# Optimization experiments

Measured on AMD Instinct MI355X. Metric: run time of the kernel, lower is better.

## Reference

```python
import jax, jax.numpy as jnp
import numpy as np

D_MODEL = 768
HEADS = 12
HEAD_DIM = D_MODEL // HEADS


def setup_inputs() -> dict:
    key = jax.random.key(0)
    ks = jax.random.split(key, 5)
    B, L = 4, 2048
    x = jax.random.normal(ks[0], (B, L, D_MODEL), dtype=jnp.float32)
    # torch nn.Linear init scale ~ 1/sqrt(fan_in); use small random weights
    s = 1.0 / np.sqrt(D_MODEL)
    W_qkv = jax.random.uniform(ks[1], (D_MODEL, 3 * D_MODEL), jnp.float32, -s, s)
    b_qkv = jax.random.uniform(ks[2], (3 * D_MODEL,), jnp.float32, -s, s)
    W_out = jax.random.uniform(ks[3], (D_MODEL, D_MODEL), jnp.float32, -s, s)
    b_out = jax.random.uniform(ks[4], (D_MODEL,), jnp.float32, -s, s)
    return {"x": x, "W_qkv": W_qkv, "b_qkv": b_qkv, "W_out": W_out, "b_out": b_out}


def reference(x, W_qkv, b_qkv, W_out, b_out):
    B, L, D = x.shape
    scale = jnp.sqrt(jnp.float32(HEAD_DIM))
    # qkv projection: [B, L, 3*D] -> [3, B, heads, L, head_dim]
    qkv = (x @ W_qkv + b_qkv).reshape(B, L, 3, HEADS, HEAD_DIM)
    qkv = jnp.transpose(qkv, (2, 0, 3, 1, 4))
    q, k, v = qkv[0], qkv[1], qkv[2]
    # full materialized attention, no mask
    scores = jnp.einsum("bhld,bhmd->bhlm", q, k) / scale  # [B, H, L, L]
    attn = jax.nn.softmax(scores, axis=-1)
    out = jnp.einsum("bhlm,bhmd->bhld", attn, v)  # [B, H, L, head_dim]
    out = jnp.transpose(out, (0, 2, 1, 3)).reshape(B, L, D)
    return out @ W_out + b_out
```

## Files before the change

### kernel.cpp

```cpp
#include <hip/hip_runtime.h>
#include <cmath>

typedef __bf16 bf16_t;
typedef __bf16 bf16x8 __attribute__((ext_vector_type(8)));
typedef __bf16 bf16x4 __attribute__((ext_vector_type(4)));
typedef short s16x4 __attribute__((ext_vector_type(4)));
typedef float f32x4 __attribute__((ext_vector_type(4)));

#define MFMA(a, b, c) __builtin_amdgcn_mfma_f32_16x16x32_bf16((a), (b), (c), 0, 0, 0)
#if __has_builtin(__builtin_amdgcn_mfma_f32_16x16x16_bf16)
#define MFMA16(a, b, c) __builtin_amdgcn_mfma_f32_16x16x16_bf16((a), (b), (c), 0, 0, 0)
#else
#define MFMA16(a, b, c)                                                              \
  __builtin_amdgcn_mfma_f32_16x16x16bf16_1k(__builtin_bit_cast(s16x4, (bf16x4)(a)), \
                                            __builtin_bit_cast(s16x4, (bf16x4)(b)), (c), 0, 0, 0)
#endif

static constexpr int D = 768;
static constexpr int L = 2048;
static constexpr int NB = 4;
static constexpr int NH = 12;
static constexpr int HD = 64;
static constexpr int M = 8192;
static constexpr int NQKV = 2304;
#define QSCALE 0.18033688011112042f

__device__ __forceinline__ void glds16(const bf16_t* g, bf16_t* l) {
  __builtin_amdgcn_global_load_lds((const __attribute__((address_space(1))) void*)g,
                                   (__attribute__((address_space(3))) void*)l, 16, 0, 0);
}

__global__ __launch_bounds__(256) void cvt_bf16_kernel(const float* __restrict__ in,
                                                       bf16_t* __restrict__ out, int n8) {
  int g = blockIdx.x * 256 + threadIdx.x;
  if (g >= n8) return;
  const float4* p = (const float4*)in + (size_t)g * 2;
  float4 a = p[0], b = p[1];
  bf16x8 v = {(__bf16)a.x, (__bf16)a.y, (__bf16)a.z, (__bf16)a.w,
              (__bf16)b.x, (__bf16)b.y, (__bf16)b.z, (__bf16)b.w};
  *(bf16x8*)(out + (size_t)g * 8) = v;
}

__global__ __launch_bounds__(256) void transpose_cvt_kernel(const float* __restrict__ in,
                                                            bf16_t* __restrict__ out,
                                                            int rows, int cols) {
  __shared__ float t[32][33];
  int c0 = blockIdx.x * 32, r0 = blockIdx.y * 32;
  int tx = threadIdx.x, ty = threadIdx.y;
  for (int i = ty; i < 32; i += 8) t[i][tx] = in[(size_t)(r0 + i) * cols + c0 + tx];
  __syncthreads();
  for (int i = ty; i < 32; i += 8) out[(size_t)(c0 + i) * rows + r0 + tx] = (__bf16)t[tx][i];
}

__global__ __launch_bounds__(256) void gemm_qkv_kernel(const bf16_t* __restrict__ A,
                                                       const bf16_t* __restrict__ Bt,
                                                       const float* __restrict__ bias,
                                                       bf16_t* __restrict__ Qo,
                                                       bf16_t* __restrict__ Ko,
                                                       bf16_t* __restrict__ Vto) {
  __shared__ __align__(16) bf16_t As[128 * 32];
  __shared__ __align__(16) bf16_t Bs[128 * 32];
  const int tid = threadIdx.x;
  const int wave = tid >> 6, lane = tid & 63;
  const int quad = lane >> 4, l16 = lane & 15;
  const int wm = (wave >> 1) * 64, wn = (wave & 1) * 64;
  const int tm = blockIdx.x * 128, tn = blockIdx.y * 128;
  const int lr = tid >> 2, lc = (tid & 3) * 8;
  const bf16_t* Ag = A + (size_t)(tm + lr) * D + lc;
  const bf16_t* Bg = Bt + (size_t)(tn + lr) * D + lc;
  bf16_t* lA0 = &As[wave * 512];
  bf16_t* lA1 = &As[2048 + wave * 512];
  bf16_t* lB0 = &Bs[wave * 512];
  bf16_t* lB1 = &Bs[2048 + wave * 512];
  f32x4 acc[4][4] = {};
  for (int kt = 0; kt < D; kt += 32) {
    __syncthreads();
    glds16(Ag + kt, lA0);
    glds16(Ag + (size_t)64 * D + kt, lA1);
    glds16(Bg + kt, lB0);
    glds16(Bg + (size_t)64 * D + kt, lB1);
    __syncthreads();
    bf16x8 af[4], bfr[4];
#pragma unroll
    for (int i = 0; i < 4; i++) af[i] = *(const bf16x8*)&As[(wm + i * 16 + l16) * 32 + quad * 8];
#pragma unroll
    for (int j = 0; j < 4; j++) bfr[j] = *(const bf16x8*)&Bs[(wn + j * 16 + l16) * 32 + quad * 8];
#pragma unroll
    for (int i = 0; i < 4; i++)
#pragma unroll
      for (int j = 0; j < 4; j++) acc[i][j] = MFMA(af[i], bfr[j], acc[i][j]);
  }
#pragma unroll
  for (int i = 0; i < 4; i++)
#pragma unroll
    for (int j = 0; j < 4; j++) {
      int n = tn + wn + j * 16 + l16;
      float bn = bias[n];
      int which = n / 768, rem = n - which * 768;
      int h = rem >> 6, d = rem & 63;
      int m0 = tm + wm + i * 16 + quad * 4;
      int b0 = m0 >> 11, l0 = m0 & 2047;
      int bh = b0 * NH + h;
      if (which == 2) {
        int l6 = l0 & 63;
        int lp = (l0 & ~63) | (((l6 >> 2) & 3) * 16) | ((l6 >> 4) * 4);
        bf16x4 w;
#pragma unroll
        for (int r2 = 0; r2 < 4; r2++) w[r2] = (__bf16)(acc[i][j][r2] + bn);
        *(bf16x4*)&Vto[((size_t)bh * HD + d) * L + lp] = w;
      } else if (which == 0) {
#pragma unroll
        for (int r2 = 0; r2 < 4; r2++)
          Qo[((size_t)bh * L + l0 + r2) * HD + d] = (__bf16)((acc[i][j][r2] + bn) * QSCALE);
      } else {
#pragma unroll
        for (int r2 = 0; r2 < 4; r2++)
          Ko[((size_t)bh * L + l0 + r2) * HD + d] = (__bf16)(acc[i][j][r2] + bn);
      }
    }
}

__global__ __launch_bounds__(256) void attn_kernel(const bf16_t* __restrict__ Q,
                                                   const bf16_t* __restrict__ K,
                                                   const bf16_t* __restrict__ Vt,
                                                   bf16_t* __restrict__ O) {
  __shared__ __align__(16) bf16_t Ks[64][72];
  __shared__ __align__(16) bf16_t Vs[64][72];
  const int tid = threadIdx.x;
  const int wave = tid >> 6, lane = tid & 63;
  const int quad = lane >> 4, l16 = lane & 15;
  const int bh = blockIdx.y;
  const int q0 = blockIdx.x * 128 + wave * 32;
  const bf16_t* Kb = K + (size_t)bh * L * HD;
  const bf16_t* Vb = Vt + (size_t)bh * HD * L;
  bf16x8 bq[2][2];
#pragma unroll
  for (int g = 0; g < 2; g++) {
    const bf16_t* Qp = Q + ((size_t)bh * L + q0 + g * 16 + l16) * HD + quad * 8;
    bq[g][0] = *(const bf16x8*)Qp;
    bq[g][1] = *(const bf16x8*)(Qp + 32);
  }
  f32x4 oacc[2][4] = {};
  float lacc[2] = {0.f, 0.f};
  const int st = tid >> 3, sc = (tid & 7) * 8;
  bf16x8 pk0 = *(const bf16x8*)(Kb + (size_t)st * HD + sc);
  bf16x8 pk1 = *(const bf16x8*)(Kb + (size_t)(st + 32) * HD + sc);
  bf16x8 pv0 = *(const bf16x8*)(Vb + (size_t)st * L + sc);
  bf16x8 pv1 = *(const bf16x8*)(Vb + (size_t)(st + 32) * L + sc);
  for (int j = 0; j < L / 64; j++) {
    __syncthreads();
    *(bf16x8*)&Ks[st][sc] = pk0;
    *(bf16x8*)&Ks[st + 32][sc] = pk1;
    *(bf16x8*)&Vs[st][sc] = pv0;
    *(bf16x8*)&Vs[st + 32][sc] = pv1;
    __syncthreads();
    if (j + 1 < L / 64) {
      int kv0n = (j + 1) * 64;
      pk0 = *(const bf16x8*)(Kb + (size_t)(kv0n + st) * HD + sc);
      pk1 = *(const bf16x8*)(Kb + (size_t)(kv0n + st + 32) * HD + sc);
      pv0 = *(const bf16x8*)(Vb + (size_t)st * L + kv0n + sc);
      pv1 = *(const bf16x8*)(Vb + (size_t)(st + 32) * L + kv0n + sc);
    }
    f32x4 s[2][4];
#pragma unroll
    for (int fn = 0; fn < 4; fn++) {
      bf16x8 ak0 = *(const bf16x8*)&Ks[fn * 16 + l16][quad * 8];
      bf16x8 ak1 = *(const bf16x8*)&Ks[fn * 16 + l16][32 + quad * 8];
#pragma unroll
      for (int g = 0; g < 2; g++) {
        f32x4 z = {};
        z = MFMA(ak0, bq[g][0], z);
        s[g][fn] = MFMA(ak1, bq[g][1], z);
      }
    }
    bf16x4 pb[2][4];
#pragma unroll
    for (int g = 0; g < 2; g++)
#pragma unroll
      for (int fn = 0; fn < 4; fn++) {
        float e0 = exp2f(s[g][fn][0]), e1 = exp2f(s[g][fn][1]);
        float e2 = exp2f(s[g][fn][2]), e3 = exp2f(s[g][fn][3]);
        lacc[g] += (e0 + e1) + (e2 + e3);
        bf16x4 w = {(__bf16)e0, (__bf16)e1, (__bf16)e2, (__bf16)e3};
        pb[g][fn] = w;
      }
#pragma unroll
    for (int fd = 0; fd < 4; fd++)
#pragma unroll
      for (int t = 0; t < 2; t++) {
        bf16x8 av2 = *(const bf16x8*)&Vs[fd * 16 + l16][quad * 16 + t * 8];
        bf16x4 av0 = {av2[0], av2[1], av2[2], av2[3]};
        bf16x4 av1 = {av2[4], av2[5], av2[6], av2[7]};
#pragma unroll
        for (int g = 0; g < 2; g++) {
          oacc[g][fd] = MFMA16(av0, pb[g][2 * t], oacc[g][fd]);
          oacc[g][fd] = MFMA16(av1, pb[g][2 * t + 1], oacc[g][fd]);
        }
      }
  }
  const int b = bh / NH, h = bh - b * NH;
#pragma unroll
  for (int g = 0; g < 2; g++) {
    float ls = lacc[g];
    ls += __shfl_xor(ls, 16, 64);
    ls += __shfl_xor(ls, 32, 64);
    float rinv = 1.f / ls;
    int row = q0 + g * 16 + l16;
    bf16_t* Op = O + ((size_t)(b * L + row)) * D + h * HD;
#pragma unroll
    for (int fd = 0; fd < 4; fd++) {
      bf16x4 w;
#pragma unroll
      for (int r = 0; r < 4; r++) w[r] = (__bf16)(oacc[g][fd][r] * rinv);
      *(bf16x4*)(Op + fd * 16 + quad * 4) = w;
    }
  }
}

__global__ __launch_bounds__(256) void gemm_out_kernel(const bf16_t* __restrict__ A,
                                                       const bf16_t* __restrict__ Bt,
                                                       const float* __restrict__ bias,
                                                       float* __restrict__ Cg) {
  __shared__ __align__(16) bf16_t As[128 * 32];
  __shared__ __align__(16) bf16_t Bs[128 * 32];
  const int tid = threadIdx.x;
  const int wave = tid >> 6, lane = tid & 63;
  const int quad = lane >> 4, l16 = lane & 15;
  const int wm = (wave >> 1) * 64, wn = (wave & 1) * 64;
  const int tm = blockIdx.x * 128, tn = blockIdx.y * 128;
  const int lr = tid >> 2, lc = (tid & 3) * 8;
  const bf16_t* Ag = A + (size_t)(tm + lr) * D + lc;
  const bf16_t* Bg = Bt + (size_t)(tn + lr) * D + lc;
  bf16_t* lA0 = &As[wave * 512];
  bf16_t* lA1 = &As[2048 + wave * 512];
  bf16_t* lB0 = &Bs[wave * 512];
  bf16_t* lB1 = &Bs[2048 + wave * 512];
  f32x4 acc[4][4] = {};
  for (int kt = 0; kt < D; kt += 32) {
    __syncthreads();
    glds16(Ag + kt, lA0);
    glds16(Ag + (size_t)64 * D + kt, lA1);
    glds16(Bg + kt, lB0);
    glds16(Bg + (size_t)64 * D + kt, lB1);
    __syncthreads();
    bf16x8 af[4], bfr[4];
#pragma unroll
    for (int i = 0; i < 4; i++) af[i] = *(const bf16x8*)&As[(wm + i * 16 + l16) * 32 + quad * 8];
#pragma unroll
    for (int j = 0; j < 4; j++) bfr[j] = *(const bf16x8*)&Bs[(wn + j * 16 + l16) * 32 + quad * 8];
#pragma unroll
    for (int i = 0; i < 4; i++)
#pragma unroll
      for (int j = 0; j < 4; j++) acc[i][j] = MFMA(af[i], bfr[j], acc[i][j]);
  }
#pragma unroll
  for (int i = 0; i < 4; i++)
#pragma unroll
    for (int j = 0; j < 4; j++) {
      int n = tn + wn + j * 16 + l16;
      float bn = bias[n];
#pragma unroll
      for (int r2 = 0; r2 < 4; r2++) {
        int m = tm + wm + i * 16 + quad * 4 + r2;
        Cg[(size_t)m * D + n] = acc[i][j][r2] + bn;
      }
    }
}

extern "C" void kernel_launch(void* const* d_in, const int* in_sizes, int n_in,
                              void* d_out, int out_size, void* d_ws, size_t ws_size,
                              hipStream_t stream) {
  const float* x = (const float*)d_in[0];
  const float* Wqkv = (const float*)d_in[1];
  const float* bqkv = (const float*)d_in[2];
  const float* Wout = (const float*)d_in[3];
  const float* bout = (const float*)d_in[4];
  float* out = (float*)d_out;

  bf16_t* xb = (bf16_t*)d_ws;
  bf16_t* wqT = xb + (size_t)M * D;
  bf16_t* woT = wqT + (size_t)NQKV * D;
  bf16_t* Qb = woT + (size_t)D * D;
  bf16_t* Kb = Qb + (size_t)M * D;
  bf16_t* Vtb = Kb + (size_t)M * D;
  bf16_t* Ob = Vtb + (size_t)M * D;

  cvt_bf16_kernel<<<(M * D / 8 + 255) / 256, 256, 0, stream>>>(x, xb, M * D / 8);
  transpose_cvt_kernel<<<dim3(NQKV / 32, D / 32), dim3(32, 8), 0, stream>>>(Wqkv, wqT, D, NQKV);
  transpose_cvt_kernel<<<dim3(D / 32, D / 32), dim3(32, 8), 0, stream>>>(Wout, woT, D, D);
  gemm_qkv_kernel<<<dim3(M / 128, NQKV / 128), 256, 0, stream>>>(xb, wqT, bqkv, Qb, Kb, Vtb);
  attn_kernel<<<dim3(L / 128, NB * NH), 256, 0, stream>>>(Qb, Kb, Vtb, Ob);
  gemm_out_kernel<<<dim3(M / 128, D / 128), 256, 0, stream>>>(Ob, woT, bout, out);
}
```

Before: 244.9 us.

## Load K/V fragments directly from global memory, dropping LDS staging and barriers

The attention kernel no longer stages K and V tiles through shared memory with two __syncthreads per iteration. Each wave now loads its MFMA operand fragments for K and V^T straight from global memory into registers. It also switches exp2f to the raw hardware exp2 builtin and requests 3 blocks per CU in launch_bounds. This removes the barrier and LDS round-trip cost, but each of the four waves now fetches the same K/V data separately, so it relies on L1/L2 hits and exposes global load latency with no explicit prefetch.

```diff
diff --git a/kernel.cpp b/kernel.cpp
--- a/kernel.cpp
+++ b/kernel.cpp
@@ -15,6 +15,8 @@
   __builtin_amdgcn_mfma_f32_16x16x16bf16_1k(__builtin_bit_cast(s16x4, (bf16x4)(a)), \
                                             __builtin_bit_cast(s16x4, (bf16x4)(b)), (c), 0, 0, 0)
 #endif
+
+#define EXP2(x) __builtin_amdgcn_exp2f(x)
 
 static constexpr int D = 768;
 static constexpr int L = 2048;
@@ -120,12 +122,10 @@
     }
 }
 
-__global__ __launch_bounds__(256) void attn_kernel(const bf16_t* __restrict__ Q,
-                                                   const bf16_t* __restrict__ K,
-                                                   const bf16_t* __restrict__ Vt,
-                                                   bf16_t* __restrict__ O) {
-  __shared__ __align__(16) bf16_t Ks[64][72];
-  __shared__ __align__(16) bf16_t Vs[64][72];
+__global__ __launch_bounds__(256, 3) void attn_kernel(const bf16_t* __restrict__ Q,
+                                                      const bf16_t* __restrict__ K,
+                                                      const bf16_t* __restrict__ Vt,
+                                                      bf16_t* __restrict__ O) {
   const int tid = threadIdx.x;
   const int wave = tid >> 6, lane = tid & 63;
   const int quad = lane >> 4, l16 = lane & 15;
@@ -142,44 +142,39 @@
   }
   f32x4 oacc[2][4] = {};
   float lacc[2] = {0.f, 0.f};
-  const int st = tid >> 3, sc = (tid & 7) * 8;
-  bf16x8 pk0 = *(const bf16x8*)(Kb + (size_t)st * HD + sc);
-  bf16x8 pk1 = *(const bf16x8*)(Kb + (size_t)(st + 32) * HD + sc);
-  bf16x8 pv0 = *(const bf16x8*)(Vb + (size_t)st * L + sc);
-  bf16x8 pv1 = *(const bf16x8*)(Vb + (size_t)(st + 32) * L + sc);
+  const bf16_t* kp = Kb + (size_t)l16 * HD + quad * 8;
+  const bf16_t* vp = Vb + (size_t)l16 * L + quad * 16;
+#pragma unroll 1
   for (int j = 0; j < L / 64; j++) {
-    __syncthreads();
-    *(bf16x8*)&Ks[st][sc] = pk0;
-    *(bf16x8*)&Ks[st + 32][sc] = pk1;
-    *(bf16x8*)&Vs[st][sc] = pv0;
-    *(bf16x8*)&Vs[st + 32][sc] = pv1;
-    __syncthreads();
-    if (j + 1 < L / 64) {
-      int kv0n = (j + 1) * 64;
-      pk0 = *(const bf16x8*)(Kb + (size_t)(kv0n + st) * HD + sc);
-      pk1 = *(const bf16x8*)(Kb + (size_t)(kv0n + st + 32) * HD + sc);
-      pv0 = *(const bf16x8*)(Vb + (size_t)st * L + kv0n + sc);
-      pv1 = *(const bf16x8*)(Vb + (size_t)(st + 32) * L + kv0n + sc);
-    }
+    bf16x8 kf[4][2], vf[4][2];
+#pragma unroll
+    for (int fd = 0; fd < 4; fd++) {
+      vf[fd][0] = *(const bf16x8*)(vp + (size_t)fd * 16 * L);
+      vf[fd][1] = *(const bf16x8*)(vp + (size_t)fd * 16 * L + 8);
+    }
+#pragma unroll
+    for (int fn = 0; fn < 4; fn++) {
+      kf[fn][0] = *(const bf16x8*)(kp + (size_t)fn * 16 * HD);
+      kf[fn][1] = *(const bf16x8*)(kp + (size_t)fn * 16 * HD + 32);
+    }
+    kp += 64 * HD;
+    vp += 64;
     f32x4 s[2][4];
 #pragma unroll
-    for (int fn = 0; fn < 4; fn++) {
-      bf16x8 ak0 = *(const bf16x8*)&Ks[fn * 16 + l16][quad * 8];
-      bf16x8 ak1 = *(const bf16x8*)&Ks[fn * 16 + l16][32 + quad * 8];
+    for (int fn = 0; fn < 4; fn++)
 #pragma unroll
       for (int g = 0; g < 2; g++) {
         f32x4 z = {};
-        z = MFMA(ak0, bq[g][0], z);
-        s[g][fn] = MFMA(ak1, bq[g][1], z);
-      }
-    }
+        z = MFMA(kf[fn][0], bq[g][0], z);
+        s[g][fn] = MFMA(kf[fn][1], bq[g][1], z);
+      }
     bf16x4 pb[2][4];
 #pragma unroll
     for (int g = 0; g < 2; g++)
 #pragma unroll
       for (int fn = 0; fn < 4; fn++) {
-        float e0 = exp2f(s[g][fn][0]), e1 = exp2f(s[g][fn][1]);
-        float e2 = exp2f(s[g][fn][2]), e3 = exp2f(s[g][fn][3]);
+        float e0 = EXP2(s[g][fn][0]), e1 = EXP2(s[g][fn][1]);
+        float e2 = EXP2(s[g][fn][2]), e3 = EXP2(s[g][fn][3]);
         lacc[g] += (e0 + e1) + (e2 + e3);
         bf16x4 w = {(__bf16)e0, (__bf16)e1, (__bf16)e2, (__bf16)e3};
         pb[g][fn] = w;
@@ -188,7 +183,7 @@
     for (int fd = 0; fd < 4; fd++)
 #pragma unroll
       for (int t = 0; t < 2; t++) {
-        bf16x8 av2 = *(const bf16x8*)&Vs[fd * 16 + l16][quad * 16 + t * 8];
+        bf16x8 av2 = vf[fd][t];
         bf16x4 av0 = {av2[0], av2[1], av2[2], av2[3]};
         bf16x4 av1 = {av2[4], av2[5], av2[6], av2[7]};
 #pragma unroll
```

Result: slower. 328.6 us (+34.2%).
